# Kernel tuning notes

Measured on AMD Instinct MI355X. Metric: run time of the kernel, lower is better.

The kernel has to match this reference:

```python
import jax, jax.numpy as jnp
import numpy as np

N_EMBD = 1024
N_HEAD = 16
HEAD_DIM = N_EMBD // N_HEAD


def setup_inputs() -> dict:
    key = jax.random.key(0)
    kx, kq, kk, kv, ko = jax.random.split(key, 5)
    B, T = 4, 2048
    x = jax.random.normal(kx, (B, T, N_EMBD), dtype=jnp.float32)
    s = N_EMBD ** -0.5
    Wq = jax.random.normal(kq, (N_EMBD, N_EMBD), dtype=jnp.float32) * s
    Wk = jax.random.normal(kk, (N_EMBD, HEAD_DIM), dtype=jnp.float32) * s
    Wv = jax.random.normal(kv, (N_EMBD, HEAD_DIM), dtype=jnp.float32) * s
    Wo = jax.random.normal(ko, (N_EMBD, N_EMBD), dtype=jnp.float32) * s
    return {"x": x, "Wq": Wq, "Wk": Wk, "Wv": Wv, "Wo": Wo}


def reference(x, Wq, Wk, Wv, Wo):
    B, T, C = x.shape
    scale = HEAD_DIM ** -0.5
    # q: [B, H, T, D]; shared k, v: [B, T, D]
    q = (x @ Wq).reshape(B, T, N_HEAD, HEAD_DIM).transpose(0, 2, 1, 3)
    k = x @ Wk
    v = x @ Wv
    # scores: [B, H, T, T] (shared K head broadcast over H)
    att = jnp.einsum('bhtd,bsd->bhts', q, k) * scale
    causal = jnp.tril(jnp.ones((T, T), dtype=bool))
    att = jnp.where(causal, att, -jnp.inf)
    att = jax.nn.softmax(att, axis=-1)
    out = jnp.einsum('bhts,bsd->bhtd', att, v)  # [B, H, T, D]
    out = out.transpose(0, 2, 1, 3).reshape(B, T, C)
    return out @ Wo
```

## Files before the change

kernel.cpp:

```cpp
#include <hip/hip_runtime.h>

typedef __attribute__((ext_vector_type(8))) short short8;
typedef __attribute__((ext_vector_type(4))) float f32x4;

__device__ __forceinline__ unsigned short f2bf(float f) {
  unsigned u = __builtin_bit_cast(unsigned, f);
  u += 0x7fffu + ((u >> 16) & 1u);
  return (unsigned short)(u >> 16);
}
__device__ __forceinline__ unsigned pack_bf2_rtz(float p0, float p1) {
  return __builtin_amdgcn_perm(__builtin_bit_cast(unsigned, p1),
                               __builtin_bit_cast(unsigned, p0), 0x07060302u);
}

#define GLDS16(g, l)                                                          \
  __builtin_amdgcn_global_load_lds(                                           \
      (const __attribute__((address_space(1))) void*)(g),                     \
      (__attribute__((address_space(3))) void*)(l), 16, 0, 0)

#define QSCALE 0.18033688011112042f

__global__ void cast_x_bf16(const float4* __restrict__ in,
                            ushort4* __restrict__ out, int n4) {
  int i = blockIdx.x * blockDim.x + threadIdx.x;
  if (i >= n4) return;
  float4 v = in[i];
  ushort4 o;
  o.x = f2bf(v.x); o.y = f2bf(v.y); o.z = f2bf(v.z); o.w = f2bf(v.w);
  out[i] = o;
}

__global__ void transpose_cvt_all(const float* __restrict__ Wq,
                                  const float* __restrict__ Wk,
                                  const float* __restrict__ Wv,
                                  const float* __restrict__ Wo,
                                  unsigned short* __restrict__ Wcat,
                                  unsigned short* __restrict__ Wot) {
  __shared__ float tile[32][33];
  const int z = blockIdx.z;
  int bx = blockIdx.x;
  const float* in;
  unsigned short* out;
  int N;
  if (z == 0)      { in = Wq; out = Wcat;               N = 1024; }
  else if (z == 1) { in = Wo; out = Wot;                N = 1024; }
  else {
    if (bx < 2)      { in = Wk; out = Wcat + 1024 * 1024; N = 64; }
    else if (bx < 4) { in = Wv; out = Wcat + 1088 * 1024; N = 64; bx -= 2; }
    else return;
  }
  const int K = 1024;
  const int n0 = bx * 32, k0 = blockIdx.y * 32;
  const int tx = threadIdx.x, ty = threadIdx.y;
#pragma unroll
  for (int i = 0; i < 4; ++i)
    tile[ty + 8 * i][tx] = in[(size_t)(k0 + ty + 8 * i) * N + n0 + tx];
  __syncthreads();
#pragma unroll
  for (int i = 0; i < 4; ++i)
    out[(size_t)(n0 + ty + 8 * i) * K + k0 + tx] = f2bf(tile[tx][ty + 8 * i]);
}

__global__ void transpose_v(const unsigned short* __restrict__ Vr,
                            unsigned short* __restrict__ Vt) {
  __shared__ unsigned short tile[32][34];
  const int t0 = blockIdx.x * 32;
  const int d0 = blockIdx.y * 32;
  const int b = blockIdx.z;
  const int tx = threadIdx.x, ty = threadIdx.y;
#pragma unroll
  for (int i = 0; i < 4; ++i)
    tile[ty + 8 * i][tx] =
        Vr[(size_t)(b * 2048 + t0 + ty + 8 * i) * 64 + d0 + tx];
  __syncthreads();
#pragma unroll
  for (int i = 0; i < 4; ++i)
    Vt[((size_t)b * 64 + d0 + ty + 8 * i) * 2048 + t0 + tx] =
        tile[tx][ty + 8 * i];
}

template <int EPI>
__global__ __launch_bounds__(256) void gemm_bt(
    const unsigned short* __restrict__ A, const unsigned short* __restrict__ Bt,
    unsigned short* __restrict__ Cq, unsigned short* __restrict__ Ck,
    unsigned short* __restrict__ Cv, float* __restrict__ Cf, int N, int K) {
  __shared__ __align__(16) unsigned short As[128 * 64];
  __shared__ __align__(16) unsigned short Bs[128 * 64];
  const int tid = threadIdx.x;
  const int w = tid >> 6, lane = tid & 63;
  const int nwg = gridDim.x * gridDim.y;
  const int lid = blockIdx.y * gridDim.x + blockIdx.x;
  const int cpx = nwg >> 3;
  const int swz = (lid & 7) * cpx + (lid >> 3);
  const int m0 = (swz / gridDim.x) * 128, n0 = (swz % gridDim.x) * 128;
  const int wm = (w >> 1) * 64, wn = (w & 1) * 64;
  const int g = lane >> 4, c = lane & 15;
  const int lr = lane >> 3, lc = (lane & 7) * 8;

  f32x4 acc[4][4] = {};

  for (int k0 = 0; k0 < K; k0 += 64) {
#pragma unroll
    for (int i = 0; i < 4; ++i) {
      int ci = w * 4 + i;
      GLDS16(A + (size_t)(m0 + ci * 8 + lr) * K + k0 + lc, As + ci * 512);
      GLDS16(Bt + (size_t)(n0 + ci * 8 + lr) * K + k0 + lc, Bs + ci * 512);
    }
    __syncthreads();
#pragma unroll
    for (int kk = 0; kk < 2; ++kk) {
      const int col = kk * 32 + g * 8;
      short8 av[4], bv[4];
#pragma unroll
      for (int mi = 0; mi < 4; ++mi)
        av[mi] = *(const short8*)(As + (wm + mi * 16 + c) * 64 + col);
#pragma unroll
      for (int ni = 0; ni < 4; ++ni)
        bv[ni] = *(const short8*)(Bs + (wn + ni * 16 + c) * 64 + col);
#pragma unroll
      for (int mi = 0; mi < 4; ++mi)
#pragma unroll
        for (int ni = 0; ni < 4; ++ni)
          acc[mi][ni] = __builtin_amdgcn_mfma_f32_16x16x32_bf16(
              av[mi], bv[ni], acc[mi][ni], 0, 0, 0);
    }
    __syncthreads();
  }

#pragma unroll
  for (int mi = 0; mi < 4; ++mi) {
#pragma unroll
    for (int ni = 0; ni < 4; ++ni) {
      f32x4 a = acc[mi][ni];
      const int col = n0 + wn + ni * 16 + c;
#pragma unroll
      for (int r = 0; r < 4; ++r) {
        const int row = m0 + wm + mi * 16 + g * 4 + r;
        float v = a[r];
        if (EPI == 0) {
          if (col < 1024)
            Cq[(size_t)row * 1024 + col] = f2bf(v * QSCALE);
          else if (col < 1088)
            Ck[(size_t)row * 64 + (col - 1024)] = f2bf(v);
          else
            Cv[(size_t)row * 64 + (col - 1088)] = f2bf(v);
        } else {
          Cf[(size_t)row * N + col] = v;
        }
      }
    }
  }
}

__global__ __launch_bounds__(1024, 8) void attn_mqa(
    const unsigned short* __restrict__ Q, const unsigned short* __restrict__ Kb,
    const unsigned short* __restrict__ Vt, unsigned short* __restrict__ Oc) {
  __shared__ __align__(16) unsigned short Kl[2][64 * 64];
  __shared__ __align__(16) unsigned short Vl[2][64 * 64];
  __shared__ __align__(16) unsigned short Pl[16][16 * 72];
  const int tid = threadIdx.x;
  const int w = tid >> 6, lane = tid & 63;
  const int bid = blockIdx.x;
  const int hq = (bid >> 2) & 3;
  const int b = bid & 3;
  const int qi16 = (bid >> 4) & 15;
  const int qt = (bid < 256) ? qi16 : 31 - qi16;
  const int h = hq * 4 + (w >> 2);
  const int wq = w & 3;
  const int g = lane >> 4, c = lane & 15;
  const int swr = (c & 7) * 8;
  const int sh = tid >> 9;
  const int st = tid & 511;
  const int srow = st >> 3;
  const int scs = ((st & 7) ^ (srow & 7)) * 8;
  const unsigned short* Kbase = Kb + (size_t)b * 2048 * 64;
  const unsigned short* Vbase = Vt + (size_t)b * 64 * 2048;
  const unsigned short* sp = sh ? Vbase + (size_t)srow * 2048 + scs
                                : Kbase + (size_t)srow * 64 + scs;
  const ptrdiff_t sstep = sh ? 64 : 4096;
  unsigned short* ld0 = (sh ? &Vl[0][0] : &Kl[0][0]) + st * 8;
  unsigned short* ld1 = (sh ? &Vl[1][0] : &Kl[1][0]) + st * 8;
  unsigned short* pw = Pl[w];
  unsigned* pd = (unsigned*)pw;

  short8 ones;
#pragma unroll
  for (int j = 0; j < 8; ++j) ones[j] = (short)0x3F80;

  const int qb = qt * 64 + wq * 16;
  const int qi = qb + c;

  short8 qf[2];
#pragma unroll
  for (int kk = 0; kk < 2; ++kk)
    qf[kk] = *(const short8*)(Q + (size_t)(b * 2048 + qb + c) * 1024 +
                              h * 64 + kk * 32 + g * 8);

  f32x4 po[4] = {};
  f32x4 lac = {};
  float m = -1e30f;

  GLDS16(sp, ld0);
  sp += sstep;
  int cur = 0;

  for (int it = 0; it <= qt; ++it) {
    __syncthreads();

    if (it < qt) {
      GLDS16(sp, cur ? ld0 : ld1);
      sp += sstep;
    }

    const unsigned short* Kt = &Kl[cur][0];
    const unsigned short* Vc = &Vl[cur][0];
    const int kv0 = it * 64;

    f32x4 s[4] = {};
    __builtin_amdgcn_s_setprio(1);
#pragma unroll
    for (int kk = 0; kk < 2; ++kk) {
      const int col = (kk * 32 + g * 8) ^ swr;
#pragma unroll
      for (int f = 0; f < 4; ++f) {
        short8 kf = *(const short8*)(Kt + (f * 16 + c) * 64 + col);
        s[f] = __builtin_amdgcn_mfma_f32_16x16x32_bf16(kf, qf[kk], s[f], 0, 0, 0);
      }
    }
    __builtin_amdgcn_s_setprio(0);

    if (it == qt) {
#pragma unroll
      for (int f = 0; f < 4; ++f)
#pragma unroll
        for (int r = 0; r < 4; ++r)
          if (kv0 + f * 16 + g * 4 + r > qi) s[f][r] = -1e30f;
    }

    const float t0 = fmaxf(fmaxf(s[0][0], s[0][1]), s[0][2]);
    const float t1 = fmaxf(fmaxf(s[0][3], s[1][0]), s[1][1]);
    const float t2 = fmaxf(fmaxf(s[1][2], s[1][3]), s[2][0]);
    const float t3 = fmaxf(fmaxf(s[2][1], s[2][2]), s[2][3]);
    const float t4 = fmaxf(fmaxf(s[3][0], s[3][1]), s[3][2]);
    const float u0 = fmaxf(fmaxf(t0, t1), t2);
    const float u1 = fmaxf(fmaxf(t3, t4), s[3][3]);
    float pm = fmaxf(u0, u1);

    if (!__all(pm <= m + 8.0f)) {
      pm = fmaxf(pm, __shfl_xor(pm, 16, 64));
      pm = fmaxf(pm, __shfl_xor(pm, 32, 64));
      const float mn = fmaxf(m, pm);
      const float al = __builtin_amdgcn_exp2f(m - mn);
      m = mn;
#pragma unroll
      for (int r = 0; r < 4; ++r) {
        const float ar = __shfl(al, g * 4 + r, 64);
        lac[r] *= ar;
#pragma unroll
        for (int fd = 0; fd < 4; ++fd) po[fd][r] *= ar;
      }
    }

#pragma unroll
    for (int f = 0; f < 4; ++f) {
      const float p0 = __builtin_amdgcn_exp2f(s[f][0] - m);
      const float p1 = __builtin_amdgcn_exp2f(s[f][1] - m);
      const float p2 = __builtin_amdgcn_exp2f(s[f][2] - m);
      const float p3 = __builtin_amdgcn_exp2f(s[f][3] - m);
      uint2 pk;
      pk.x = pack_bf2_rtz(p0, p1);
      pk.y = pack_bf2_rtz(p2, p3);
      *(uint2*)(pd + c * 36 + f * 8 + g * 2) = pk;
    }

    __builtin_amdgcn_s_setprio(1);
#pragma unroll
    for (int kk = 0; kk < 2; ++kk) {
      short8 pa = *(const short8*)(pw + c * 72 + kk * 32 + g * 8);
      lac = __builtin_amdgcn_mfma_f32_16x16x32_bf16(pa, ones, lac, 0, 0, 0);
      const int col = (kk * 32 + g * 8) ^ swr;
#pragma unroll
      for (int fd = 0; fd < 4; ++fd) {
        short8 vf = *(const short8*)(Vc + (fd * 16 + c) * 64 + col);
        po[fd] = __builtin_amdgcn_mfma_f32_16x16x32_bf16(pa, vf, po[fd], 0, 0, 0);
      }
    }
    __builtin_amdgcn_s_setprio(0);
    cur ^= 1;
  }

#pragma unroll
  for (int r = 0; r < 4; ++r) {
    const float inv = __builtin_amdgcn_rcpf(lac[r]);
    const int trow = qb + g * 4 + r;
#pragma unroll
    for (int fd = 0; fd < 4; ++fd)
      Oc[(size_t)(b * 2048 + trow) * 1024 + h * 64 + fd * 16 + c] =
          f2bf(po[fd][r] * inv);
  }
}

extern "C" void kernel_launch(void* const* d_in, const int* in_sizes, int n_in,
                              void* d_out, int out_size, void* d_ws,
                              size_t ws_size, hipStream_t stream) {
  const float* x = (const float*)d_in[0];
  const float* Wq = (const float*)d_in[1];
  const float* Wk = (const float*)d_in[2];
  const float* Wv = (const float*)d_in[3];
  const float* Wo = (const float*)d_in[4];
  float* out = (float*)d_out;

  char* ws = (char*)d_ws;
  unsigned short* xb   = (unsigned short*)ws;
  unsigned short* Qb   = (unsigned short*)(ws + (size_t)(16u << 20));
  unsigned short* Attn = (unsigned short*)(ws + (size_t)(32u << 20));
  unsigned short* Wcat = (unsigned short*)(ws + (size_t)(48u << 20));
  unsigned short* Wot  = (unsigned short*)(ws + (size_t)(48u << 20) + 2359296);
  unsigned short* Kb   = (unsigned short*)(ws + (size_t)(48u << 20) + 2359296 + 2097152);
  unsigned short* Vtb  = (unsigned short*)(ws + (size_t)(48u << 20) + 2359296 + 2097152 + 1048576);
  unsigned short* Vrow = Attn;

  cast_x_bf16<<<8192, 256, 0, stream>>>((const float4*)x, (ushort4*)xb, 2097152);
  transpose_cvt_all<<<dim3(32, 32, 3), dim3(32, 8), 0, stream>>>(Wq, Wk, Wv, Wo,
                                                                 Wcat, Wot);

  gemm_bt<0><<<dim3(9, 64), 256, 0, stream>>>(xb, Wcat, Qb, Kb, Vrow, nullptr,
                                              1152, 1024);
  transpose_v<<<dim3(64, 2, 4), dim3(32, 8), 0, stream>>>(Vrow, Vtb);

  attn_mqa<<<512, 1024, 0, stream>>>(Qb, Kb, Vtb, Attn);

  gemm_bt<1><<<dim3(8, 64), 256, 0, stream>>>(Attn, Wot, nullptr, nullptr,
                                              nullptr, out, 1024, 1024);
}
```

Measured before the change: 153.8 us.

## Process two 16-row query sub-tiles per wave in MQA attention

Each wave now handles 32 query rows (two 16-row sub-tiles) instead of 16. The block shrinks to 512 threads covering 2 heads by 128 queries, with each thread loading both a K and a V chunk. Every K/V fragment read from LDS now feeds two MFMAs, halving LDS traffic per FLOP, and the causal mask is applied per sub-tile. The cost is higher register pressure (doubled accumulators), fewer waves per block, and a coarser causal tile that adds some masked work on the diagonal.

```diff
diff --git a/kernel.cpp b/kernel.cpp
--- a/kernel.cpp
+++ b/kernel.cpp
@@ -152,34 +152,28 @@
   }
 }
 
-__global__ __launch_bounds__(1024, 8) void attn_mqa(
+__global__ __launch_bounds__(512, 4) void attn_mqa(
     const unsigned short* __restrict__ Q, const unsigned short* __restrict__ Kb,
     const unsigned short* __restrict__ Vt, unsigned short* __restrict__ Oc) {
   __shared__ __align__(16) unsigned short Kl[2][64 * 64];
   __shared__ __align__(16) unsigned short Vl[2][64 * 64];
-  __shared__ __align__(16) unsigned short Pl[16][16 * 72];
+  __shared__ __align__(16) unsigned short Pl[8][32 * 72];
   const int tid = threadIdx.x;
   const int w = tid >> 6, lane = tid & 63;
   const int bid = blockIdx.x;
-  const int hq = (bid >> 2) & 3;
   const int b = bid & 3;
-  const int qi16 = (bid >> 4) & 15;
-  const int qt = (bid < 256) ? qi16 : 31 - qi16;
-  const int h = hq * 4 + (w >> 2);
+  const int hp = (bid >> 2) & 7;
+  const int qidx = (bid >> 5) & 7;
+  const int half = (bid >> 8) & 1;
+  const int qt = half ? (15 - qidx) : qidx;
+  const int h = hp * 2 + (w >> 2);
   const int wq = w & 3;
   const int g = lane >> 4, c = lane & 15;
   const int swr = (c & 7) * 8;
-  const int sh = tid >> 9;
-  const int st = tid & 511;
-  const int srow = st >> 3;
-  const int scs = ((st & 7) ^ (srow & 7)) * 8;
+  const int srow = tid >> 3;
+  const int scs = ((tid & 7) ^ (srow & 7)) * 8;
   const unsigned short* Kbase = Kb + (size_t)b * 2048 * 64;
   const unsigned short* Vbase = Vt + (size_t)b * 64 * 2048;
-  const unsigned short* sp = sh ? Vbase + (size_t)srow * 2048 + scs
-                                : Kbase + (size_t)srow * 64 + scs;
-  const ptrdiff_t sstep = sh ? 64 : 4096;
-  unsigned short* ld0 = (sh ? &Vl[0][0] : &Kl[0][0]) + st * 8;
-  unsigned short* ld1 = (sh ? &Vl[1][0] : &Kl[1][0]) + st * 8;
   unsigned short* pw = Pl[w];
   unsigned* pd = (unsigned*)pw;
 
@@ -187,36 +181,42 @@
 #pragma unroll
   for (int j = 0; j < 8; ++j) ones[j] = (short)0x3F80;
 
-  const int qb = qt * 64 + wq * 16;
-  const int qi = qb + c;
-
-  short8 qf[2];
-#pragma unroll
-  for (int kk = 0; kk < 2; ++kk)
-    qf[kk] = *(const short8*)(Q + (size_t)(b * 2048 + qb + c) * 1024 +
-                              h * 64 + kk * 32 + g * 8);
-
-  f32x4 po[4] = {};
-  f32x4 lac = {};
-  float m = -1e30f;
-
-  GLDS16(sp, ld0);
-  sp += sstep;
+  const int qb = qt * 128 + wq * 32;
+
+  short8 qf[2][2];
+#pragma unroll
+  for (int u = 0; u < 2; ++u)
+#pragma unroll
+    for (int kk = 0; kk < 2; ++kk)
+      qf[u][kk] = *(const short8*)(Q + (size_t)(b * 2048 + qb + u * 16 + c) *
+                                           1024 + h * 64 + kk * 32 + g * 8);
+
+  f32x4 po[2][4] = {};
+  f32x4 lac[2] = {};
+  float m[2] = {-1e30f, -1e30f};
+
+  GLDS16(Kbase + (size_t)srow * 64 + scs, &Kl[0][0] + tid * 8);
+  GLDS16(Vbase + (size_t)srow * 2048 + scs, &Vl[0][0] + tid * 8);
+  const unsigned short* kpf = Kbase + (size_t)(64 + srow) * 64 + scs;
+  const unsigned short* vpf = Vbase + (size_t)srow * 2048 + 64 + scs;
   int cur = 0;
-
-  for (int it = 0; it <= qt; ++it) {
+  const int nit = 2 * qt + 2;
+
+  for (int it = 0; it < nit; ++it) {
     __syncthreads();
 
-    if (it < qt) {
-      GLDS16(sp, cur ? ld0 : ld1);
-      sp += sstep;
+    if (it < nit - 1) {
+      GLDS16(kpf, &Kl[cur ^ 1][0] + tid * 8);
+      GLDS16(vpf, &Vl[cur ^ 1][0] + tid * 8);
+      kpf += 64 * 64;
+      vpf += 64;
     }
 
     const unsigned short* Kt = &Kl[cur][0];
     const unsigned short* Vc = &Vl[cur][0];
     const int kv0 = it * 64;
 
-    f32x4 s[4] = {};
+    f32x4 s[2][4] = {};
     __builtin_amdgcn_s_setprio(1);
 #pragma unroll
     for (int kk = 0; kk < 2; ++kk) {
@@ -224,65 +224,83 @@
 #pragma unroll
       for (int f = 0; f < 4; ++f) {
         short8 kf = *(const short8*)(Kt + (f * 16 + c) * 64 + col);
-        s[f] = __builtin_amdgcn_mfma_f32_16x16x32_bf16(kf, qf[kk], s[f], 0, 0, 0);
+        s[0][f] = __builtin_amdgcn_mfma_f32_16x16x32_bf16(kf, qf[0][kk],
+                                                          s[0][f], 0, 0, 0);
+        s[1][f] = __builtin_amdgcn_mfma_f32_16x16x32_bf16(kf, qf[1][kk],
+                                                          s[1][f], 0, 0, 0);
       }
     }
     __builtin_amdgcn_s_setprio(0);
 
-    if (it == qt) {
-#pragma unroll
-      for (int f = 0; f < 4; ++f)
-#pragma unroll
-        for (int r = 0; r < 4; ++r)
-          if (kv0 + f * 16 + g * 4 + r > qi) s[f][r] = -1e30f;
-    }
-
-    const float t0 = fmaxf(fmaxf(s[0][0], s[0][1]), s[0][2]);
-    const float t1 = fmaxf(fmaxf(s[0][3], s[1][0]), s[1][1]);
-    const float t2 = fmaxf(fmaxf(s[1][2], s[1][3]), s[2][0]);
-    const float t3 = fmaxf(fmaxf(s[2][1], s[2][2]), s[2][3]);
-    const float t4 = fmaxf(fmaxf(s[3][0], s[3][1]), s[3][2]);
-    const float u0 = fmaxf(fmaxf(t0, t1), t2);
-    const float u1 = fmaxf(fmaxf(t3, t4), s[3][3]);
-    float pm = fmaxf(u0, u1);
-
-    if (!__all(pm <= m + 8.0f)) {
-      pm = fmaxf(pm, __shfl_xor(pm, 16, 64));
-      pm = fmaxf(pm, __shfl_xor(pm, 32, 64));
-      const float mn = fmaxf(m, pm);
-      const float al = __builtin_amdgcn_exp2f(m - mn);
-      m = mn;
-#pragma unroll
-      for (int r = 0; r < 4; ++r) {
-        const float ar = __shfl(al, g * 4 + r, 64);
-        lac[r] *= ar;
-#pragma unroll
-        for (int fd = 0; fd < 4; ++fd) po[fd][r] *= ar;
-      }
-    }
-
-#pragma unroll
-    for (int f = 0; f < 4; ++f) {
-      const float p0 = __builtin_amdgcn_exp2f(s[f][0] - m);
-      const float p1 = __builtin_amdgcn_exp2f(s[f][1] - m);
-      const float p2 = __builtin_amdgcn_exp2f(s[f][2] - m);
-      const float p3 = __builtin_amdgcn_exp2f(s[f][3] - m);
-      uint2 pk;
-      pk.x = pack_bf2_rtz(p0, p1);
-      pk.y = pack_bf2_rtz(p2, p3);
-      *(uint2*)(pd + c * 36 + f * 8 + g * 2) = pk;
+    float pm[2];
+#pragma unroll
+    for (int u = 0; u < 2; ++u) {
+      if (kv0 + 63 > qb + u * 16) {
+        const int qi = qb + u * 16 + c;
+#pragma unroll
+        for (int f = 0; f < 4; ++f)
+#pragma unroll
+          for (int r = 0; r < 4; ++r)
+            if (kv0 + f * 16 + g * 4 + r > qi) s[u][f][r] = -1e30f;
+      }
+      const float t0 = fmaxf(fmaxf(s[u][0][0], s[u][0][1]), s[u][0][2]);
+      const float t1 = fmaxf(fmaxf(s[u][0][3], s[u][1][0]), s[u][1][1]);
+      const float t2 = fmaxf(fmaxf(s[u][1][2], s[u][1][3]), s[u][2][0]);
+      const float t3 = fmaxf(fmaxf(s[u][2][1], s[u][2][2]), s[u][2][3]);
+      const float t4 = fmaxf(fmaxf(s[u][3][0], s[u][3][1]), s[u][3][2]);
+      const float u0 = fmaxf(fmaxf(t0, t1), t2);
+      const float u1 = fmaxf(fmaxf(t3, t4), s[u][3][3]);
+      pm[u] = fmaxf(u0, u1);
+    }
+
+    if (!__all(pm[0] <= m[0] + 8.0f && pm[1] <= m[1] + 8.0f)) {
+#pragma unroll
+      for (int u = 0; u < 2; ++u) {
+        float pmu = fmaxf(pm[u], __shfl_xor(pm[u], 16, 64));
+        pmu = fmaxf(pmu, __shfl_xor(pmu, 32, 64));
+        const float mn = fmaxf(m[u], pmu);
+        const float al = __builtin_amdgcn_exp2f(m[u] - mn);
+        m[u] = mn;
+#pragma unroll
+        for (int r = 0; r < 4; ++r) {
+          const float ar = __shfl(al, g * 4 + r, 64);
+          lac[u][r] *= ar;
+#pragma unroll
+          for (int fd = 0; fd < 4; ++fd) po[u][fd][r] *= ar;
+        }
+      }
+    }
+
+#pragma unroll
+    for (int u = 0; u < 2; ++u) {
+#pragma unroll
+      for (int f = 0; f < 4; ++f) {
+        const float p0 = __builtin_amdgcn_exp2f(s[u][f][0] - m[u]);
+        const float p1 = __builtin_amdgcn_exp2f(s[u][f][1] - m[u]);
+        const float p2 = __builtin_amdgcn_exp2f(s[u][f][2] - m[u]);
+        const float p3 = __builtin_amdgcn_exp2f(s[u][f][3] - m[u]);
+        uint2 pk;
+        pk.x = pack_bf2_rtz(p0, p1);
+        pk.y = pack_bf2_rtz(p2, p3);
+        *(uint2*)(pd + (u * 16 + c) * 36 + f * 8 + g * 2) = pk;
+      }
     }
 
     __builtin_amdgcn_s_setprio(1);
 #pragma unroll
     for (int kk = 0; kk < 2; ++kk) {
-      short8 pa = *(const short8*)(pw + c * 72 + kk * 32 + g * 8);
-      lac = __builtin_amdgcn_mfma_f32_16x16x32_bf16(pa, ones, lac, 0, 0, 0);
+      short8 pa0 = *(const short8*)(pw + c * 72 + kk * 32 + g * 8);
+      short8 pa1 = *(const short8*)(pw + (16 + c) * 72 + kk * 32 + g * 8);
+      lac[0] = __builtin_amdgcn_mfma_f32_16x16x32_bf16(pa0, ones, lac[0], 0, 0, 0);
+      lac[1] = __builtin_amdgcn_mfma_f32_16x16x32_bf16(pa1, ones, lac[1], 0, 0, 0);
       const int col = (kk * 32 + g * 8) ^ swr;
 #pragma unroll
       for (int fd = 0; fd < 4; ++fd) {
         short8 vf = *(const short8*)(Vc + (fd * 16 + c) * 64 + col);
-        po[fd] = __builtin_amdgcn_mfma_f32_16x16x32_bf16(pa, vf, po[fd], 0, 0, 0);
+        po[0][fd] = __builtin_amdgcn_mfma_f32_16x16x32_bf16(pa0, vf, po[0][fd],
+                                                            0, 0, 0);
+        po[1][fd] = __builtin_amdgcn_mfma_f32_16x16x32_bf16(pa1, vf, po[1][fd],
+                                                            0, 0, 0);
       }
     }
     __builtin_amdgcn_s_setprio(0);
@@ -290,13 +308,16 @@
   }
 
 #pragma unroll
-  for (int r = 0; r < 4; ++r) {
-    const float inv = __builtin_amdgcn_rcpf(lac[r]);
-    const int trow = qb + g * 4 + r;
-#pragma unroll
-    for (int fd = 0; fd < 4; ++fd)
-      Oc[(size_t)(b * 2048 + trow) * 1024 + h * 64 + fd * 16 + c] =
-          f2bf(po[fd][r] * inv);
+  for (int u = 0; u < 2; ++u) {
+#pragma unroll
+    for (int r = 0; r < 4; ++r) {
+      const float inv = __builtin_amdgcn_rcpf(lac[u][r]);
+      const int trow = qb + u * 16 + g * 4 + r;
+#pragma unroll
+      for (int fd = 0; fd < 4; ++fd)
+        Oc[(size_t)(b * 2048 + trow) * 1024 + h * 64 + fd * 16 + c] =
+            f2bf(po[u][fd][r] * inv);
+    }
   }
 }
 
@@ -328,7 +349,7 @@
                                               1152, 1024);
   transpose_v<<<dim3(64, 2, 4), dim3(32, 8), 0, stream>>>(Vrow, Vtb);
 
-  attn_mqa<<<512, 1024, 0, stream>>>(Qb, Kb, Vtb, Attn);
+  attn_mqa<<<512, 512, 0, stream>>>(Qb, Kb, Vtb, Attn);
 
   gemm_bt<1><<<dim3(8, 64), 256, 0, stream>>>(Attn, Wot, nullptr, nullptr,
                                               nullptr, out, 1024, 1024);
```

Result: no change. 156.5 us (+1.8%).
